# Kernel tuning notes

Hardware: AMD Instinct MI355X
Metric: run time of the kernel (lower is better)

## Reference

```python
import math
import jax, jax.numpy as jnp
import numpy as np

B_SZ, N_TOK, D_INNER, S_STATE = 4, 1024, 384, 16
DT_MAX = 0.15


def setup_inputs() -> dict:
    key = jax.random.key(0)
    ks = jax.random.split(key, 10)
    dt_init = math.log(math.exp(0.1) - 1.0)  # softplus^-1(0.1)
    x = jax.random.normal(ks[0], (B_SZ, N_TOK, D_INNER), dtype=jnp.float32)
    dt_self_W = jax.random.uniform(ks[1], (D_INNER, D_INNER), minval=-1e-4, maxval=1e-4)
    dt_self_b = jnp.full((D_INNER,), dt_init, dtype=jnp.float32)
    dt_diff_W = jax.random.uniform(ks[2], (D_INNER, D_INNER), minval=-1e-4, maxval=1e-4)
    dt_diff_b = jnp.full((D_INNER,), dt_init, dtype=jnp.float32)
    B_W = jax.random.normal(ks[3], (D_INNER, S_STATE)) / math.sqrt(D_INNER)
    C_real_W = jax.random.normal(ks[4], (D_INNER, S_STATE)) / math.sqrt(D_INNER)
    C_imag_W = jax.random.normal(ks[5], (D_INNER, S_STATE)) / math.sqrt(D_INNER)
    D_param = jnp.ones((D_INNER,), dtype=jnp.float32)
    A_log = jnp.broadcast_to(jnp.log(jnp.arange(1, S_STATE + 1, dtype=jnp.float32))[None, :], (D_INNER, S_STATE))
    lap = jnp.array([[0.0, 1.0, 0.0], [1.0, -4.0, 1.0], [0.0, 1.0, 0.0]], dtype=jnp.float32) * 0.1
    conv_w = jnp.broadcast_to(lap[None, None], (D_INNER, 1, 3, 3)) + 0.01 * jax.random.normal(ks[6], (D_INNER, 1, 3, 3))
    reaction_alpha = 0.01 * jax.random.normal(ks[7], (1, 1, D_INNER, 1))
    reaction_beta = 0.01 * jax.random.normal(ks[8], (1, 1, D_INNER, 1))
    return {
        'x': x, 'dt_self_W': dt_self_W, 'dt_self_b': dt_self_b,
        'dt_diff_W': dt_diff_W, 'dt_diff_b': dt_diff_b,
        'B_W': B_W, 'C_real_W': C_real_W, 'C_imag_W': C_imag_W,
        'D_param': D_param, 'A_log': A_log, 'conv_w': conv_w,
        'reaction_alpha': reaction_alpha, 'reaction_beta': reaction_beta,
        'K_steps': 2,
    }


def _laplacian(h, conv_w, H, W):
    # h: (B, N, D, S) -> depthwise 3x3 conv with replicate pad over the HxW grid
    B, N, D, S = h.shape
    hs = h.transpose(0, 3, 2, 1).reshape(B * S, D, H, W)
    hp = jnp.pad(hs, ((0, 0), (0, 0), (1, 1), (1, 1)), mode='edge')
    lap = jax.lax.conv_general_dilated(
        hp, conv_w, window_strides=(1, 1), padding='VALID',
        feature_group_count=D, dimension_numbers=('NCHW', 'OIHW', 'NCHW'))
    return lap.reshape(B, S, D, N).transpose(0, 3, 2, 1)


def reference(x, dt_self_W, dt_self_b, dt_diff_W, dt_diff_b, B_W, C_real_W,
              C_imag_W, D_param, A_log, conv_w, reaction_alpha, reaction_beta,
              K_steps):
    B, N, D = x.shape
    H = Wg = int(math.sqrt(N))
    A = -jax.nn.softplus(A_log)  # (D, S)
    delta_s = jnp.minimum(jax.nn.softplus(x @ dt_self_W.T + dt_self_b), DT_MAX)[..., None]
    delta_d = jnp.minimum(jax.nn.softplus(x @ dt_diff_W.T + dt_diff_b), DT_MAX)[..., None]
    B_mat = x @ B_W          # (B, N, S)
    C_real = x @ C_real_W    # (B, N, S)
    C_imag = x @ C_imag_W    # (B, N, S)
    mamba_input = jnp.einsum('bnd,bns->bnds', x, B_mat)
    h_real = mamba_input
    h_imag = jnp.zeros_like(h_real)
    dt = 1.0 / K_steps
    A_exp = A[None, None]  # (1,1,D,S)
    for _ in range(K_steps):
        f1_real = delta_s * (A_exp * h_real + mamba_input)
        f1_imag = delta_s * (A_exp * h_imag)
        lap_real = _laplacian(h_real, conv_w, H, Wg)
        lap_imag = _laplacian(h_imag, conv_w, H, Wg)
        f2_real = delta_d * -lap_imag
        f2_imag = delta_d * lap_real
        reaction_scale = reaction_alpha - reaction_beta * (h_real ** 2 + h_imag ** 2)
        h_real = h_real + dt * (f1_real + f2_real + h_real * reaction_scale)
        h_imag = h_imag + dt * (f1_imag + f2_imag + h_imag * reaction_scale)
    y = (jnp.einsum('bnds,bns->bnd', h_real, C_real)
         + jnp.einsum('bnds,bns->bnd', h_imag, C_imag)
         + x * D_param)
    return y
```

## Files before the change

### kernel.cpp

```cpp
#include <hip/hip_runtime.h>
#include <hip/hip_fp16.h>
#include <math.h>

#define B_SZ    4
#define N_TOKC  1024
#define D_INNER 384
#define S_STATE 16
#define DT_MAX_V 0.15f
#define PLANE   (B_SZ * N_TOKC)
#define DN      ((size_t)B_SZ * D_INNER * N_TOKC)

typedef __attribute__((ext_vector_type(8))) short bf16x8;
typedef __attribute__((ext_vector_type(4))) float f32x4;

__device__ __forceinline__ float softplusf(float z) {
    return fmaxf(z, 0.f) + log1pf(expf(-fabsf(z)));
}

__device__ __forceinline__ unsigned short f2bf(float f) {
    unsigned u = __float_as_uint(f);
    unsigned r = (u + 0x7FFFu + ((u >> 16) & 1u)) >> 16;
    return (unsigned short)r;
}

__device__ __forceinline__ unsigned packh2(float a, float b) {
    __half2 h = __floats2half2_rn(a, b);
    union { __half2 h; unsigned u; } c; c.h = h; return c.u;
}
__device__ __forceinline__ __half2 uph2(unsigned u) {
    union { unsigned u; __half2 h; } c; c.u = u; return c.h;
}

__device__ __forceinline__ size_t frag_off(int T, int kb, int q, int l16) {
    return ((size_t)((T * 12 + kb) * 4 + q)) * 128 + l16 * 8;
}

__device__ __forceinline__ bf16x8 pack8(const float* v) {
    bf16x8 o;
#pragma unroll
    for (int e = 0; e < 8; e++) o[e] = (short)f2bf(v[e]);
    return o;
}

__global__ __launch_bounds__(256) void k_prep(
    const float* __restrict__ x, const float* __restrict__ Ws, const float* __restrict__ Wd,
    const float* __restrict__ BW, const float* __restrict__ CrW, const float* __restrict__ CiW,
    const float* __restrict__ A_log,
    float* __restrict__ x_t, unsigned short* __restrict__ xp,
    unsigned short* __restrict__ Wdtp, unsigned short* __restrict__ Wbcp,
    float* __restrict__ A_tab)
{
    const int t = threadIdx.x;
    const int bx = blockIdx.x;
    if (bx < 1536) {
        __shared__ __align__(16) float tile[32][36];
        const int tok0 = (bx & 127) * 32;
        const int d0   = (bx >> 7) * 32;
        const int b = tok0 >> 10, n0 = tok0 & 1023;
        {
            const int r = t >> 3, c4 = (t & 7) * 4;
            const float4 v = *(const float4*)(x + (size_t)(tok0 + r) * D_INNER + d0 + c4);
            tile[r][c4 + 0] = v.x; tile[r][c4 + 1] = v.y;
            tile[r][c4 + 2] = v.z; tile[r][c4 + 3] = v.w;
        }
        __syncthreads();
        {
            const int dr = t >> 3, n4 = (t & 7) * 4;
            float4 o;
            o.x = tile[n4 + 0][dr]; o.y = tile[n4 + 1][dr];
            o.z = tile[n4 + 2][dr]; o.w = tile[n4 + 3][dr];
            *(float4*)(x_t + ((size_t)(b * D_INNER + d0 + dr)) * N_TOKC + n0 + n4) = o;
        }
        if (t < 128) {
            const int tt = t >> 6, q = (t >> 4) & 3, l16 = t & 15;
            const int row = tt * 16 + l16;
            float v[8];
#pragma unroll
            for (int e = 0; e < 8; e++) v[e] = tile[row][q * 8 + e];
            *(bf16x8*)(xp + frag_off((tok0 >> 4) + tt, d0 >> 5, q, l16)) = pack8(v);
        }
    } else if (bx < 1584) {
        const int vv = bx - 1536;
        const int mat = vv >= 24;
        const int dt16 = mat ? vv - 24 : vv;
        const float* W = mat ? Wd : Ws;
        unsigned short* dst = Wdtp + (size_t)mat * 147456;
#pragma unroll
        for (int it = 0; it < 3; it++) {
            const int item = t + it * 256;
            const int l16 = item & 15, q = (item >> 4) & 3, kb = item >> 6;
            const float* src = W + (size_t)(dt16 * 16 + l16) * D_INNER + kb * 32 + q * 8;
            float v[8];
            const float4 v0 = *(const float4*)(src);
            const float4 v1 = *(const float4*)(src + 4);
            v[0] = v0.x; v[1] = v0.y; v[2] = v0.z; v[3] = v0.w;
            v[4] = v1.x; v[5] = v1.y; v[6] = v1.z; v[7] = v1.w;
            *(bf16x8*)(dst + frag_off(dt16, kb, q, l16)) = pack8(v);
        }
    } else if (bx < 1587) {
        const int m = bx - 1584;
        const float* W2 = (m == 0) ? BW : ((m == 1) ? CrW : CiW);
#pragma unroll
        for (int it = 0; it < 3; it++) {
            const int item = t + it * 256;
            const int l16 = item & 15, q = (item >> 4) & 3, kb = item >> 6;
            float v[8];
#pragma unroll
            for (int e = 0; e < 8; e++)
                v[e] = W2[(size_t)(kb * 32 + q * 8 + e) * S_STATE + l16];
            *(bf16x8*)(Wbcp + (size_t)m * 6144 + frag_off(0, kb, q, l16)) = pack8(v);
        }
    } else {
        for (int i = t; i < D_INNER * S_STATE; i += 256)
            A_tab[i] = -softplusf(A_log[i]);
    }
}

__global__ __launch_bounds__(256) void k_gemm(
    const unsigned short* __restrict__ xp, const unsigned short* __restrict__ Wdtp,
    const unsigned short* __restrict__ Wbcp,
    const float* __restrict__ bs, const float* __restrict__ bd,
    unsigned* __restrict__ dsdd_t,
    float* __restrict__ Bm_t, unsigned* __restrict__ cri_t)
{
    const int wave = threadIdx.x >> 6;
    const int lane = threadIdx.x & 63;
    const int quad = lane >> 4, l16 = lane & 15;

    if (blockIdx.x < 384) {
        const int dbase = (blockIdx.x >> 6) * 64;
        const int tbase = (blockIdx.x & 63) * 64;
        const int wd = (wave & 1) * 32;
        const int wt = (wave >> 1) * 32;
        const int dT0 = (dbase + wd) >> 4;
        const int tT0 = (tbase + wt) >> 4;

        f32x4 acc[2][2][2];
#pragma unroll
        for (int m = 0; m < 2; m++)
#pragma unroll
            for (int i = 0; i < 2; i++)
#pragma unroll
                for (int j = 0; j < 2; j++) acc[m][i][j] = (f32x4)0.f;

        bf16x8 a0[2][2], b0[2];
#pragma unroll
        for (int m = 0; m < 2; m++)
#pragma unroll
            for (int i = 0; i < 2; i++)
                a0[m][i] = *(const bf16x8*)(Wdtp + (size_t)m * 147456
                                            + frag_off(dT0 + i, 0, quad, l16));
#pragma unroll
        for (int j = 0; j < 2; j++)
            b0[j] = *(const bf16x8*)(xp + frag_off(tT0 + j, 0, quad, l16));

#pragma unroll 2
        for (int kb = 0; kb < 12; kb++) {
            bf16x8 a1[2][2], b1[2];
            const int kn = (kb < 11) ? kb + 1 : 11;
#pragma unroll
            for (int m = 0; m < 2; m++)
#pragma unroll
                for (int i = 0; i < 2; i++)
                    a1[m][i] = *(const bf16x8*)(Wdtp + (size_t)m * 147456
                                                + frag_off(dT0 + i, kn, quad, l16));
#pragma unroll
            for (int j = 0; j < 2; j++)
                b1[j] = *(const bf16x8*)(xp + frag_off(tT0 + j, kn, quad, l16));

#pragma unroll
            for (int m = 0; m < 2; m++)
#pragma unroll
                for (int i = 0; i < 2; i++)
#pragma unroll
                    for (int j = 0; j < 2; j++)
                        acc[m][i][j] = __builtin_amdgcn_mfma_f32_16x16x32_bf16(
                            a0[m][i], b0[j], acc[m][i][j], 0, 0, 0);

#pragma unroll
            for (int m = 0; m < 2; m++)
#pragma unroll
                for (int i = 0; i < 2; i++) a0[m][i] = a1[m][i];
#pragma unroll
            for (int j = 0; j < 2; j++) b0[j] = b1[j];
        }

#pragma unroll
        for (int i = 0; i < 2; i++)
#pragma unroll
            for (int j = 0; j < 2; j++) {
                const int tok = tbase + wt + j * 16 + l16;
                const int bb = tok >> 10, n = tok & 1023;
#pragma unroll
                for (int reg = 0; reg < 4; reg++) {
                    const int d = dbase + wd + i * 16 + quad * 4 + reg;
                    const float vs = fminf(softplusf(acc[0][i][j][reg] + bs[d]), DT_MAX_V);
                    const float vd = fminf(softplusf(acc[1][i][j][reg] + bd[d]), DT_MAX_V);
                    dsdd_t[((size_t)(bb * D_INNER + d)) * N_TOKC + n] = packh2(vs, vd);
                }
            }
    } else {
        const int tT = (blockIdx.x - 384) * 4 + wave;
        f32x4 acc[3];
#pragma unroll
        for (int m = 0; m < 3; m++) acc[m] = (f32x4)0.f;

#pragma unroll 1
        for (int kb = 0; kb < 12; kb++) {
            const bf16x8 b = *(const bf16x8*)(xp + frag_off(tT, kb, quad, l16));
#pragma unroll
            for (int m = 0; m < 3; m++) {
                const bf16x8 a = *(const bf16x8*)(Wbcp + (size_t)m * 6144
                                                  + frag_off(0, kb, quad, l16));
                acc[m] = __builtin_amdgcn_mfma_f32_16x16x32_bf16(a, b, acc[m], 0, 0, 0);
            }
        }

        const int tok = tT * 16 + l16;
#pragma unroll
        for (int reg = 0; reg < 4; reg++) {
            const int s = quad * 4 + reg;
            Bm_t [(size_t)s * PLANE + tok] = acc[0][reg];
            cri_t[(size_t)s * PLANE + tok] = packh2(acc[1][reg], acc[2][reg]);
        }
    }
}

#define PSTRIDE 33
#define PSIZE   (PSTRIDE * 32)

__global__ __launch_bounds__(256) void k_ssm(
    const float* __restrict__ x_t, const float* __restrict__ conv_w, const float* __restrict__ A_tab,
    const float* __restrict__ ralpha, const float* __restrict__ rbeta, const float* __restrict__ Dp,
    const unsigned* __restrict__ dsdd_t,
    const float* __restrict__ Bm_t, const unsigned* __restrict__ cri_t,
    float* __restrict__ y_part)
{
    const int d  = blockIdx.x;
    const int b  = blockIdx.y;
    const int t  = threadIdx.x;
    const int c  = t & 31;
    const int g  = t >> 5;
    const int r0 = g * 4;

    __shared__ unsigned pl[6 * PSIZE];

    __half2 wh[9];
#pragma unroll
    for (int i = 0; i < 9; i++) wh[i] = __float2half2_rn(conv_w[d * 9 + i]);
    const float alpha = ralpha[d];
    const float beta  = rbeta[d];
    const float Dv    = Dp[d];

    const size_t base_dn = ((size_t)(b * D_INNER + d)) * N_TOKC;
    const size_t base_sn = (size_t)b * N_TOKC;

    float xv[4], dsv[4], ddv[4];
#pragma unroll
    for (int k = 0; k < 4; k++) {
        const int n = (r0 + k) * 32 + c;
        xv[k] = x_t[base_dn + n];
        const __half2 dd = uph2(dsdd_t[base_dn + n]);
        dsv[k] = __low2float(dd);
        ddv[k] = __high2float(dd);
    }

    int tapw[6][3];
    {
        const int cm = (c > 0)  ? c - 1 : 0;
        const int cp = (c < 31) ? c + 1 : 31;
        const int rtop = (r0 > 0)  ? r0 - 1 : 0;
        const int rbot = (r0 < 28) ? r0 + 4 : 31;
        int rowb[6];
        rowb[0] = rtop * PSTRIDE;
#pragma unroll
        for (int k = 0; k < 4; k++) rowb[k + 1] = (r0 + k) * PSTRIDE;
        rowb[5] = rbot * PSTRIDE;
#pragma unroll
        for (int rr = 0; rr < 6; rr++) {
            tapw[rr][0] = rowb[rr] + cm;
            tapw[rr][1] = rowb[rr] + c;
            tapw[rr][2] = rowb[rr] + cp;
        }
    }
    const int ws0 = r0 * PSTRIDE + c;

    float yp[4] = { 0.f, 0.f, 0.f, 0.f };

#pragma unroll 1
    for (int sg = 0; sg < 4; sg++) {
        float A[4];
#pragma unroll
        for (int s = 0; s < 4; s++) A[s] = A_tab[d * S_STATE + sg * 4 + s];

        float Bmf[4][4];
#pragma unroll
        for (int k = 0; k < 4; k++) {
            const int n = (r0 + k) * 32 + c;
#pragma unroll
            for (int s = 0; s < 4; s++)
                Bmf[k][s] = Bm_t[(size_t)(sg * 4 + s) * PLANE + base_sn + n];
        }

#pragma unroll
        for (int p = 0; p < 2; p++)
#pragma unroll
            for (int k = 0; k < 4; k++)
                pl[p * PSIZE + ws0 + k * PSTRIDE]
                    = packh2(xv[k] * Bmf[k][2 * p], xv[k] * Bmf[k][2 * p + 1]);
        __syncthreads();

#pragma unroll
        for (int p = 0; p < 2; p++) {
            __half2 tp[6][3];
#pragma unroll
            for (int rr = 0; rr < 6; rr++)
#pragma unroll
                for (int j = 0; j < 3; j++)
                    tp[rr][j] = uph2(pl[p * PSIZE + tapw[rr][j]]);
#pragma unroll
            for (int k = 0; k < 4; k++) {
                __half2 ac = __float2half2_rn(0.f);
#pragma unroll
                for (int a = 0; a < 3; a++)
#pragma unroll
                    for (int j = 0; j < 3; j++)
                        ac = __hfma2(wh[a * 3 + j], tp[k + a][j], ac);
                const float lap[2] = { __low2float(ac), __high2float(ac) };
#pragma unroll
                for (int e = 0; e < 2; e++) {
                    const int s = 2 * p + e;
                    const float u   = xv[k] * Bmf[k][s];
                    const float f1r = dsv[k] * fmaf(A[s], u, u);
                    const float rs  = fmaf(-beta, u * u, alpha);
                    const float nhr = u + 0.5f * (f1r + u * rs);
                    const float nhi = 0.5f * ddv[k] * lap[e];
                    pl[(2 + s) * PSIZE + ws0 + k * PSTRIDE] = packh2(nhr, nhi);
                }
            }
        }
        __syncthreads();

#pragma unroll
        for (int s = 0; s < 4; s++) {
            __half2 cri[4];
#pragma unroll
            for (int k = 0; k < 4; k++)
                cri[k] = uph2(cri_t[(size_t)(sg * 4 + s) * PLANE + base_sn + (r0 + k) * 32 + c]);
            __half2 tp[6][3];
#pragma unroll
            for (int rr = 0; rr < 6; rr++)
#pragma unroll
                for (int j = 0; j < 3; j++)
                    tp[rr][j] = uph2(pl[(2 + s) * PSIZE + tapw[rr][j]]);
#pragma unroll
            for (int k = 0; k < 4; k++) {
                __half2 ac = __float2half2_rn(0.f);
#pragma unroll
                for (int a = 0; a < 3; a++)
#pragma unroll
                    for (int j = 0; j < 3; j++)
                        ac = __hfma2(wh[a * 3 + j], tp[k + a][j], ac);
                const float lapr = __low2float(ac);
                const float lapi = __high2float(ac);
                const float hrv = __low2float(tp[k + 1][1]);
                const float hiv = __high2float(tp[k + 1][1]);
                const float u   = xv[k] * Bmf[k][s];
                const float f1r = dsv[k] * fmaf(A[s], hrv, u);
                const float f1i = dsv[k] * (A[s] * hiv);
                const float f2r = -ddv[k] * lapi;
                const float f2i =  ddv[k] * lapr;
                const float q   = fmaf(hrv, hrv, hiv * hiv);
                const float rs  = fmaf(-beta, q, alpha);
                const float nhr = hrv + 0.5f * (f1r + f2r + hrv * rs);
                const float nhi = hiv + 0.5f * (f1i + f2i + hiv * rs);
                yp[k] = fmaf(nhr, __low2float(cri[k]), yp[k]);
                yp[k] = fmaf(nhi, __high2float(cri[k]), yp[k]);
            }
        }
    }

#pragma unroll
    for (int k = 0; k < 4; k++)
        y_part[base_dn + (r0 + k) * 32 + c] = fmaf(xv[k], Dv, yp[k]);
}

__global__ __launch_bounds__(256) void k_reduce(
    const float* __restrict__ y_part, float* __restrict__ y)
{
    const int d0 = blockIdx.x * 32;
    const int n0 = blockIdx.y * 32;
    const int b  = blockIdx.z;
    const int t  = threadIdx.x;
    __shared__ __align__(16) float tile[32][36];

    const int dr = t >> 3, nc4 = (t & 7) * 4;
    const float4 v = *(const float4*)(y_part
        + ((size_t)(b * D_INNER + d0 + dr)) * N_TOKC + n0 + nc4);
    tile[dr][nc4 + 0] = v.x; tile[dr][nc4 + 1] = v.y;
    tile[dr][nc4 + 2] = v.z; tile[dr][nc4 + 3] = v.w;
    __syncthreads();

    const int nr = t >> 3, dc4 = (t & 7) * 4;
    float4 o;
    o.x = tile[dc4 + 0][nr];
    o.y = tile[dc4 + 1][nr];
    o.z = tile[dc4 + 2][nr];
    o.w = tile[dc4 + 3][nr];
    *(float4*)(y + ((size_t)(b * N_TOKC + n0 + nr)) * D_INNER + d0 + dc4) = o;
}

extern "C" void kernel_launch(void* const* d_in, const int* in_sizes, int n_in,
                              void* d_out, int out_size, void* d_ws, size_t ws_size,
                              hipStream_t stream)
{
    const float* x    = (const float*)d_in[0];
    const float* Ws   = (const float*)d_in[1];
    const float* bsb  = (const float*)d_in[2];
    const float* Wd   = (const float*)d_in[3];
    const float* bdb  = (const float*)d_in[4];
    const float* BW   = (const float*)d_in[5];
    const float* CrW  = (const float*)d_in[6];
    const float* CiW  = (const float*)d_in[7];
    const float* Dp   = (const float*)d_in[8];
    const float* Alog = (const float*)d_in[9];
    const float* cw   = (const float*)d_in[10];
    const float* ra   = (const float*)d_in[11];
    const float* rb   = (const float*)d_in[12];
    float* y = (float*)d_out;

    float* ws = (float*)d_ws;
    unsigned* dsdd_t = (unsigned*)ws;
    float* x_t    = ws + DN;
    float* Bm_t   = x_t + DN;
    unsigned* cri_t = (unsigned*)(Bm_t + (size_t)S_STATE * PLANE);
    float* A_tab  = (float*)(cri_t + (size_t)S_STATE * PLANE);
    float* y_part = A_tab + (size_t)D_INNER * S_STATE;

    unsigned short* xp   = (unsigned short*)(y_part + DN);
    unsigned short* Wdtp = xp + (size_t)256 * 12 * 4 * 128;
    unsigned short* Wbcp = Wdtp + (size_t)2 * 147456;

    k_prep<<<dim3(1588), 256, 0, stream>>>(x, Ws, Wd, BW, CrW, CiW, Alog,
                                           x_t, xp, Wdtp, Wbcp, A_tab);
    k_gemm<<<dim3(448), 256, 0, stream>>>(xp, Wdtp, Wbcp, bsb, bdb,
                                          dsdd_t, Bm_t, cri_t);
    k_ssm<<<dim3(D_INNER, B_SZ), 256, 0, stream>>>(x_t, cw, A_tab, ra, rb, Dp,
                                                   dsdd_t, Bm_t, cri_t, y_part);
    k_reduce<<<dim3(12, 32, 4), 256, 0, stream>>>(y_part, y);
}
```

Before: 161.9 us.

## Pack B and C projections as fp16 pairs and vectorize SSM shared-memory planes

The GEMM now stores B_mat as packed half2 pairs of adjacent states and C real/imag as uint2 covering two states, which halves the bytes k_ssm reads per block. In k_ssm, shared-memory planes become uint2 so each tap load fetches two states at once, and the first-stage input u = x*B is computed in half precision. The goal is fewer global and LDS load instructions per state. The cost is lower precision for B_mat and u, plus 64-bit LDS accesses that may hit different bank-conflict patterns.

```diff
diff --git a/kernel.cpp b/kernel.cpp
--- a/kernel.cpp
+++ b/kernel.cpp
@@ -29,6 +29,9 @@
 }
 __device__ __forceinline__ __half2 uph2(unsigned u) {
     union { unsigned u; __half2 h; } c; c.u = u; return c.h;
+}
+__device__ __forceinline__ unsigned h2u(__half2 h) {
+    union { __half2 h; unsigned u; } c; c.h = h; return c.u;
 }
 
 __device__ __forceinline__ size_t frag_off(int T, int kb, int q, int l16) {
@@ -121,7 +124,7 @@
     const unsigned short* __restrict__ Wbcp,
     const float* __restrict__ bs, const float* __restrict__ bd,
     unsigned* __restrict__ dsdd_t,
-    float* __restrict__ Bm_t, unsigned* __restrict__ cri_t)
+    unsigned* __restrict__ Bmp, uint2* __restrict__ crip)
 {
     const int wave = threadIdx.x >> 6;
     const int lane = threadIdx.x & 63;
@@ -218,10 +221,14 @@
 
         const int tok = tT * 16 + l16;
 #pragma unroll
-        for (int reg = 0; reg < 4; reg++) {
-            const int s = quad * 4 + reg;
-            Bm_t [(size_t)s * PLANE + tok] = acc[0][reg];
-            cri_t[(size_t)s * PLANE + tok] = packh2(acc[1][reg], acc[2][reg]);
+        for (int pp = 0; pp < 2; pp++) {
+            const int sp = quad * 2 + pp;
+            const int re = pp * 2;
+            Bmp[(size_t)sp * PLANE + tok] = packh2(acc[0][re], acc[0][re + 1]);
+            uint2 cw2;
+            cw2.x = packh2(acc[1][re],     acc[2][re]);
+            cw2.y = packh2(acc[1][re + 1], acc[2][re + 1]);
+            crip[(size_t)sp * PLANE + tok] = cw2;
         }
     }
 }
@@ -233,7 +240,7 @@
     const float* __restrict__ x_t, const float* __restrict__ conv_w, const float* __restrict__ A_tab,
     const float* __restrict__ ralpha, const float* __restrict__ rbeta, const float* __restrict__ Dp,
     const unsigned* __restrict__ dsdd_t,
-    const float* __restrict__ Bm_t, const unsigned* __restrict__ cri_t,
+    const unsigned* __restrict__ Bmp, const uint2* __restrict__ crip,
     float* __restrict__ y_part)
 {
     const int d  = blockIdx.x;
@@ -243,7 +250,8 @@
     const int g  = t >> 5;
     const int r0 = g * 4;
 
-    __shared__ unsigned pl[6 * PSIZE];
+    __shared__ uint2 pl0[PSIZE];
+    __shared__ uint2 pl1[2][PSIZE];
 
     __half2 wh[9];
 #pragma unroll
@@ -256,10 +264,12 @@
     const size_t base_sn = (size_t)b * N_TOKC;
 
     float xv[4], dsv[4], ddv[4];
+    __half2 xvh[4];
 #pragma unroll
     for (int k = 0; k < 4; k++) {
         const int n = (r0 + k) * 32 + c;
         xv[k] = x_t[base_dn + n];
+        xvh[k] = __float2half2_rn(xv[k]);
         const __half2 dd = uph2(dsdd_t[base_dn + n]);
         dsv[k] = __low2float(dd);
         ddv[k] = __high2float(dd);
@@ -293,89 +303,111 @@
 #pragma unroll
         for (int s = 0; s < 4; s++) A[s] = A_tab[d * S_STATE + sg * 4 + s];
 
-        float Bmf[4][4];
+        __half2 bmp[4][2];
 #pragma unroll
         for (int k = 0; k < 4; k++) {
             const int n = (r0 + k) * 32 + c;
 #pragma unroll
-            for (int s = 0; s < 4; s++)
-                Bmf[k][s] = Bm_t[(size_t)(sg * 4 + s) * PLANE + base_sn + n];
-        }
-
-#pragma unroll
-        for (int p = 0; p < 2; p++)
-#pragma unroll
-            for (int k = 0; k < 4; k++)
-                pl[p * PSIZE + ws0 + k * PSTRIDE]
-                    = packh2(xv[k] * Bmf[k][2 * p], xv[k] * Bmf[k][2 * p + 1]);
+            for (int pp = 0; pp < 2; pp++)
+                bmp[k][pp] = uph2(Bmp[(size_t)(sg * 2 + pp) * PLANE + base_sn + n]);
+        }
+
+#pragma unroll
+        for (int k = 0; k < 4; k++) {
+            const __half2 u01 = __hmul2(xvh[k], bmp[k][0]);
+            const __half2 u23 = __hmul2(xvh[k], bmp[k][1]);
+            pl0[ws0 + k * PSTRIDE] = make_uint2(h2u(u01), h2u(u23));
+        }
         __syncthreads();
 
-#pragma unroll
-        for (int p = 0; p < 2; p++) {
-            __half2 tp[6][3];
+        {
+            uint2 tp[6][3];
 #pragma unroll
             for (int rr = 0; rr < 6; rr++)
 #pragma unroll
                 for (int j = 0; j < 3; j++)
-                    tp[rr][j] = uph2(pl[p * PSIZE + tapw[rr][j]]);
+                    tp[rr][j] = pl0[tapw[rr][j]];
 #pragma unroll
             for (int k = 0; k < 4; k++) {
-                __half2 ac = __float2half2_rn(0.f);
+                __half2 ac01 = __float2half2_rn(0.f);
+                __half2 ac23 = __float2half2_rn(0.f);
 #pragma unroll
                 for (int a = 0; a < 3; a++)
 #pragma unroll
-                    for (int j = 0; j < 3; j++)
-                        ac = __hfma2(wh[a * 3 + j], tp[k + a][j], ac);
-                const float lap[2] = { __low2float(ac), __high2float(ac) };
-#pragma unroll
-                for (int e = 0; e < 2; e++) {
-                    const int s = 2 * p + e;
-                    const float u   = xv[k] * Bmf[k][s];
+                    for (int j = 0; j < 3; j++) {
+                        ac01 = __hfma2(wh[a * 3 + j], uph2(tp[k + a][j].x), ac01);
+                        ac23 = __hfma2(wh[a * 3 + j], uph2(tp[k + a][j].y), ac23);
+                    }
+                const __half2 uc01 = uph2(tp[k + 1][1].x);
+                const __half2 uc23 = uph2(tp[k + 1][1].y);
+                const float uu[4]  = { __low2float(uc01), __high2float(uc01),
+                                       __low2float(uc23), __high2float(uc23) };
+                const float lap[4] = { __low2float(ac01), __high2float(ac01),
+                                       __low2float(ac23), __high2float(ac23) };
+                unsigned w[4];
+#pragma unroll
+                for (int s = 0; s < 4; s++) {
+                    const float u   = uu[s];
                     const float f1r = dsv[k] * fmaf(A[s], u, u);
                     const float rs  = fmaf(-beta, u * u, alpha);
                     const float nhr = u + 0.5f * (f1r + u * rs);
-                    const float nhi = 0.5f * ddv[k] * lap[e];
-                    pl[(2 + s) * PSIZE + ws0 + k * PSTRIDE] = packh2(nhr, nhi);
+                    const float nhi = 0.5f * ddv[k] * lap[s];
+                    w[s] = packh2(nhr, nhi);
                 }
+                pl1[0][ws0 + k * PSTRIDE] = make_uint2(w[0], w[1]);
+                pl1[1][ws0 + k * PSTRIDE] = make_uint2(w[2], w[3]);
             }
         }
         __syncthreads();
 
 #pragma unroll
-        for (int s = 0; s < 4; s++) {
-            __half2 cri[4];
+        for (int pp = 0; pp < 2; pp++) {
+            uint2 cr2[4];
 #pragma unroll
             for (int k = 0; k < 4; k++)
-                cri[k] = uph2(cri_t[(size_t)(sg * 4 + s) * PLANE + base_sn + (r0 + k) * 32 + c]);
-            __half2 tp[6][3];
+                cr2[k] = crip[(size_t)(sg * 2 + pp) * PLANE + base_sn + (r0 + k) * 32 + c];
+            uint2 tp[6][3];
 #pragma unroll
             for (int rr = 0; rr < 6; rr++)
 #pragma unroll
                 for (int j = 0; j < 3; j++)
-                    tp[rr][j] = uph2(pl[(2 + s) * PSIZE + tapw[rr][j]]);
+                    tp[rr][j] = pl1[pp][tapw[rr][j]];
 #pragma unroll
             for (int k = 0; k < 4; k++) {
-                __half2 ac = __float2half2_rn(0.f);
+                __half2 acE = __float2half2_rn(0.f);
+                __half2 acO = __float2half2_rn(0.f);
 #pragma unroll
                 for (int a = 0; a < 3; a++)
 #pragma unroll
-                    for (int j = 0; j < 3; j++)
-                        ac = __hfma2(wh[a * 3 + j], tp[k + a][j], ac);
-                const float lapr = __low2float(ac);
-                const float lapi = __high2float(ac);
-                const float hrv = __low2float(tp[k + 1][1]);
-                const float hiv = __high2float(tp[k + 1][1]);
-                const float u   = xv[k] * Bmf[k][s];
-                const float f1r = dsv[k] * fmaf(A[s], hrv, u);
-                const float f1i = dsv[k] * (A[s] * hiv);
-                const float f2r = -ddv[k] * lapi;
-                const float f2i =  ddv[k] * lapr;
-                const float q   = fmaf(hrv, hrv, hiv * hiv);
-                const float rs  = fmaf(-beta, q, alpha);
-                const float nhr = hrv + 0.5f * (f1r + f2r + hrv * rs);
-                const float nhi = hiv + 0.5f * (f1i + f2i + hiv * rs);
-                yp[k] = fmaf(nhr, __low2float(cri[k]), yp[k]);
-                yp[k] = fmaf(nhi, __high2float(cri[k]), yp[k]);
+                    for (int j = 0; j < 3; j++) {
+                        acE = __hfma2(wh[a * 3 + j], uph2(tp[k + a][j].x), acE);
+                        acO = __hfma2(wh[a * 3 + j], uph2(tp[k + a][j].y), acO);
+                    }
+                const __half2 hE = uph2(tp[k + 1][1].x);
+                const __half2 hO = uph2(tp[k + 1][1].y);
+#pragma unroll
+                for (int e = 0; e < 2; e++) {
+                    const int s = pp * 2 + e;
+                    const __half2 hh = e ? hO : hE;
+                    const __half2 ac = e ? acO : acE;
+                    const float hrv  = __low2float(hh);
+                    const float hiv  = __high2float(hh);
+                    const float lapr = __low2float(ac);
+                    const float lapi = __high2float(ac);
+                    const float u    = xv[k] * (e ? __high2float(bmp[k][pp])
+                                                  : __low2float(bmp[k][pp]));
+                    const float f1r = dsv[k] * fmaf(A[s], hrv, u);
+                    const float f1i = dsv[k] * (A[s] * hiv);
+                    const float f2r = -ddv[k] * lapi;
+                    const float f2i =  ddv[k] * lapr;
+                    const float q   = fmaf(hrv, hrv, hiv * hiv);
+                    const float rs  = fmaf(-beta, q, alpha);
+                    const float nhr = hrv + 0.5f * (f1r + f2r + hrv * rs);
+                    const float nhi = hiv + 0.5f * (f1i + f2i + hiv * rs);
+                    const __half2 cri = uph2(e ? cr2[k].y : cr2[k].x);
+                    yp[k] = fmaf(nhr, __low2float(cri), yp[k]);
+                    yp[k] = fmaf(nhi, __high2float(cri), yp[k]);
+                }
             }
         }
     }
@@ -432,9 +464,9 @@
     float* ws = (float*)d_ws;
     unsigned* dsdd_t = (unsigned*)ws;
     float* x_t    = ws + DN;
-    float* Bm_t   = x_t + DN;
-    unsigned* cri_t = (unsigned*)(Bm_t + (size_t)S_STATE * PLANE);
-    float* A_tab  = (float*)(cri_t + (size_t)S_STATE * PLANE);
+    unsigned* Bmp = (unsigned*)(x_t + DN);
+    uint2* crip   = (uint2*)(Bmp + (size_t)8 * PLANE);
+    float* A_tab  = (float*)(crip + (size_t)8 * PLANE);
     float* y_part = A_tab + (size_t)D_INNER * S_STATE;
 
     unsigned short* xp   = (unsigned short*)(y_part + DN);
@@ -444,8 +476,8 @@
     k_prep<<<dim3(1588), 256, 0, stream>>>(x, Ws, Wd, BW, CrW, CiW, Alog,
                                            x_t, xp, Wdtp, Wbcp, A_tab);
     k_gemm<<<dim3(448), 256, 0, stream>>>(xp, Wdtp, Wbcp, bsb, bdb,
-                                          dsdd_t, Bm_t, cri_t);
+                                          dsdd_t, Bmp, crip);
     k_ssm<<<dim3(D_INNER, B_SZ), 256, 0, stream>>>(x_t, cw, A_tab, ra, rb, Dp,
-                                                   dsdd_t, Bm_t, cri_t, y_part);
+                                                   dsdd_t, Bmp, crip, y_part);
     k_reduce<<<dim3(12, 32, 4), 256, 0, stream>>>(y_part, y);
 }
```

Measured after the change: 159.9 us. Within noise of the previous version (-1.2%).
